# Performance work log

Hardware: AMD Instinct MI355X
Metric: run time of the kernel (lower is better)

Reference implementation:

```python
import jax, jax.numpy as jnp
import numpy as np

DIM = 576
HEADS = 8
AGENT = 49
GRID_SIZE = 5
ORDER = 3
BN_EPS = 1e-5


def _kan_grid():
    h = 2.0 / GRID_SIZE  # grid_range [-1, 1]
    return jnp.arange(-ORDER, GRID_SIZE + ORDER + 1, dtype=jnp.float32) * h - 1.0


def _bsplines(x, grid):
    # x: (M, in) -> (M, in, GRID_SIZE + ORDER) Cox-de Boor B-spline bases (efficient-kan)
    xe = x[..., None]
    b = ((xe >= grid[:-1]) & (xe < grid[1:])).astype(x.dtype)
    for k in range(1, ORDER + 1):
        b = ((xe - grid[:-(k + 1)]) / (grid[k:-1] - grid[:-(k + 1)]) * b[..., :-1]
             + (grid[k + 1:] - xe) / (grid[k + 1:] - grid[1:-k]) * b[..., 1:])
    return b


def setup_inputs() -> dict:
    key = jax.random.key(0)
    ks = jax.random.split(key, 16)
    b, H, W = 32, 28, 28
    n, c = H * W, DIM
    nrm = lambda k, shape, std=0.02: jax.random.normal(k, shape, jnp.float32) * std
    return {
        "x": jax.random.normal(ks[0], (b, n, c), jnp.float32),
        "H": H,
        "W": W,
        "Wq": nrm(ks[1], (c, c)),
        "Wkv": nrm(ks[2], (2 * c, c)),
        "an_bias": nrm(ks[3], (HEADS, AGENT, 7, 7)),
        "na_bias": nrm(ks[4], (HEADS, AGENT, 7, 7)),
        "ah_bias": nrm(ks[5], (1, HEADS, AGENT, H, 1)),
        "aw_bias": nrm(ks[6], (1, HEADS, AGENT, 1, W)),
        "ha_bias": nrm(ks[7], (1, HEADS, H, 1, AGENT)),
        "wa_bias": nrm(ks[8], (1, HEADS, 1, W, AGENT)),
        "dwc_w": nrm(ks[9], (c, 1, 3, 3), 0.1),
        "dwc_b": jnp.zeros((c,), jnp.float32),
        "bn_gamma": jnp.ones((c,), jnp.float32),
        "bn_beta": jnp.zeros((c,), jnp.float32),
        "bn_mean": jnp.zeros((c,), jnp.float32),
        "bn_var": jnp.ones((c,), jnp.float32),
        "base_weight": nrm(ks[10], (c, c)),
        "spline_weight": nrm(ks[11], (c, c, GRID_SIZE + ORDER)),
        "spline_scaler": jnp.ones((c, c), jnp.float32),
    }


def reference(x, H, W, Wq, Wkv, an_bias, na_bias, ah_bias, aw_bias, ha_bias, wa_bias,
              dwc_w, dwc_b, bn_gamma, bn_beta, bn_mean, bn_var,
              base_weight, spline_weight, spline_scaler):
    b, n, c = x.shape
    h, hd = HEADS, c // HEADS
    scale = hd ** -0.5
    q = x @ Wq.T                       # (b,n,c)
    kv = x @ Wkv.T                     # (b,n,2c)  (sr_ratio == 1)
    k, v = kv[..., :c], kv[..., c:]
    # agent tokens: AdaptiveAvgPool2d(28x28 -> 7x7) == exact 4x4 mean pooling
    p = int(AGENT ** 0.5)
    agent = q.reshape(b, p, H // p, p, W // p, c).mean(axis=(2, 4)).reshape(b, AGENT, c)
    qh = q.reshape(b, n, h, hd).transpose(0, 2, 1, 3)       # (b,h,n,hd)
    kh = k.reshape(b, n, h, hd).transpose(0, 2, 1, 3)
    vh = v.reshape(b, n, h, hd).transpose(0, 2, 1, 3)
    ah = agent.reshape(b, AGENT, h, hd).transpose(0, 2, 1, 3)  # (b,h,A,hd)
    # stage 1: agent tokens attend to k/v (bilinear-upsampled 7x7 bias + separable bias)
    pb1 = jax.image.resize(an_bias, (h, AGENT, H, W), "bilinear").reshape(1, h, AGENT, n)
    pb2 = (ah_bias + aw_bias).reshape(1, h, AGENT, n)
    agent_attn = jax.nn.softmax(jnp.einsum("bhad,bhnd->bhan", ah * scale, kh) + pb1 + pb2, axis=-1)
    agent_v = jnp.einsum("bhan,bhnd->bhad", agent_attn, vh)    # (b,h,A,hd)
    # stage 2: queries attend to agent tokens
    ab1 = jax.image.resize(na_bias, (h, AGENT, H, W), "bilinear").reshape(1, h, AGENT, n).transpose(0, 1, 3, 2)
    ab2 = (ha_bias + wa_bias).reshape(1, h, n, AGENT)
    q_attn = jax.nn.softmax(jnp.einsum("bhnd,bhad->bhna", qh * scale, ah) + ab1 + ab2, axis=-1)
    out = jnp.einsum("bhna,bhad->bhnd", q_attn, agent_v).transpose(0, 2, 1, 3).reshape(b, n, c)
    # depthwise-conv + BN(eval) + ReLU residual on v
    vimg = v.transpose(0, 2, 1).reshape(b, c, H, W)
    y = jax.lax.conv_general_dilated(vimg, dwc_w, (1, 1), "SAME",
                                     feature_group_count=c,
                                     dimension_numbers=("NCHW", "OIHW", "NCHW"))
    y = y + dwc_b[None, :, None, None]
    scale_bn = (bn_gamma / jnp.sqrt(bn_var + BN_EPS))[None, :, None, None]
    y = (y - bn_mean[None, :, None, None]) * scale_bn + bn_beta[None, :, None, None]
    y = jax.nn.relu(y).reshape(b, c, n).transpose(0, 2, 1)
    out = out + y
    # KANLinear projection: silu base branch + B-spline branch
    xf = out.reshape(b * n, c)
    bases = _bsplines(xf, _kan_grid())                           # (M, in, 8)
    scaled = spline_weight * spline_scaler[..., None]            # (out, in, 8)
    proj = jax.nn.silu(xf) @ base_weight.T + jnp.einsum("mik,oik->mo", bases, scaled)
    return proj.reshape(b, n, c)
```

## Files before the change

### kernel.cpp

```cpp
#include <hip/hip_runtime.h>
#include <hip/hip_bf16.h>
#include <math.h>

#define B_ 32
#define N_ 784
#define C_ 576
#define H_ 28
#define W_ 28
#define HEADS_ 8
#define HD_ 72
#define AGENT_ 49
#define M_ (B_ * N_)
#define KTOT_ 5184
#define QKVW_ 1728
#define SCALE_ 0.11785113019775793f

#define SWZ(row, chunk) (((row) << 5) + ((((chunk) ^ (((row) >> 1) & 3))) << 3))

typedef unsigned short ushort_t;
typedef __attribute__((ext_vector_type(8))) unsigned short u16x8;
typedef __attribute__((ext_vector_type(8))) __bf16 bf16x8;
typedef __attribute__((ext_vector_type(4))) float f32x4;
typedef __attribute__((ext_vector_type(4))) unsigned u32x4;

__device__ __forceinline__ ushort_t f2bf(float f) {
  union { float f; unsigned u; } v; v.f = f;
  unsigned r = v.u + 0x7fffu + ((v.u >> 16) & 1u);
  return (ushort_t)(r >> 16);
}
__device__ __forceinline__ float bf2f(ushort_t u) {
  union { unsigned u; float f; } v; v.u = ((unsigned)u) << 16;
  return v.f;
}
__device__ __forceinline__ unsigned pack2(float lo, float hi) {
  __bf16 a = (__bf16)lo, b = (__bf16)hi;
  unsigned short ua = __builtin_bit_cast(unsigned short, a);
  unsigned short ub = __builtin_bit_cast(unsigned short, b);
  return (unsigned)ua | ((unsigned)ub << 16);
}

__global__ __launch_bounds__(256) void convert_x_kernel(
    const float* __restrict__ x, ushort_t* __restrict__ xbf) {
  const int total8 = M_ * C_ / 8;
  for (int i = blockIdx.x * 256 + threadIdx.x; i < total8; i += gridDim.x * 256) {
    f32x4 a = *(const f32x4*)(x + i * 8);
    f32x4 b = *(const f32x4*)(x + i * 8 + 4);
    u16x8 o;
    o[0]=f2bf(a[0]); o[1]=f2bf(a[1]); o[2]=f2bf(a[2]); o[3]=f2bf(a[3]);
    o[4]=f2bf(b[0]); o[5]=f2bf(b[1]); o[6]=f2bf(b[2]); o[7]=f2bf(b[3]);
    *(u16x8*)(xbf + i * 8) = o;
  }
}

__global__ __launch_bounds__(256) void pack_w_kernel(
    const float* __restrict__ Wq, const float* __restrict__ Wkv,
    ushort_t* __restrict__ wbf) {
  int total = QKVW_ * C_;
  for (int i = blockIdx.x * 256 + threadIdx.x; i < total; i += gridDim.x * 256) {
    int j = i / C_, k = i % C_;
    float v = (j < C_) ? Wq[(size_t)j * C_ + k] : Wkv[(size_t)(j - C_) * C_ + k];
    wbf[i] = f2bf(v);
  }
}

__global__ __launch_bounds__(256) void pack_b_kernel(
    const float* __restrict__ base_w, const float* __restrict__ spline_w,
    const float* __restrict__ spline_s, ushort_t* __restrict__ bpackb) {
  int o = blockIdx.x;
  for (int j = threadIdx.x; j < KTOT_; j += 256) {
    float v;
    if (j < C_) {
      v = base_w[(size_t)o * C_ + j];
    } else {
      int jj = j - C_;
      int i = jj >> 3, kk = jj & 7;
      v = spline_w[((size_t)o * C_ + i) * 8 + kk] * spline_s[(size_t)o * C_ + i];
    }
    bpackb[(size_t)o * KTOT_ + j] = f2bf(v);
  }
}

__device__ __forceinline__ float bilerp7(const float* __restrict__ Bsrc, int y, int x) {
  float sy = y * 0.25f - 0.375f;
  float sx = x * 0.25f - 0.375f;
  float fy0 = floorf(sy), fx0 = floorf(sx);
  int y0 = (int)fy0, x0 = (int)fx0;
  float fy = sy - fy0, fx = sx - fx0;
  int y0c = min(6, max(0, y0)), y1c = min(6, max(0, y0 + 1));
  int x0c = min(6, max(0, x0)), x1c = min(6, max(0, x0 + 1));
  float v00 = Bsrc[y0c * 7 + x0c], v01 = Bsrc[y0c * 7 + x1c];
  float v10 = Bsrc[y1c * 7 + x0c], v11 = Bsrc[y1c * 7 + x1c];
  return (1.f - fy) * ((1.f - fx) * v00 + fx * v01)
       + fy * ((1.f - fx) * v10 + fx * v11);
}

__global__ __launch_bounds__(256) void bias_kernel(
    const float* __restrict__ an_bias, const float* __restrict__ na_bias,
    const float* __restrict__ ah_bias, const float* __restrict__ aw_bias,
    const float* __restrict__ ha_bias, const float* __restrict__ wa_bias,
    float* __restrict__ abias, float* __restrict__ qbias) {
  int idx = blockIdx.x * 256 + threadIdx.x;
  if (idx >= HEADS_ * AGENT_ * N_) return;
  int n = idx % N_;
  int ha = idx / N_;
  int h = ha / AGENT_, a = ha % AGENT_;
  int y = n / W_, x = n % W_;
  float pb1 = bilerp7(an_bias + (size_t)ha * 49, y, x);
  float pb2 = ah_bias[ha * H_ + y] + aw_bias[ha * W_ + x];
  abias[(size_t)ha * N_ + n] = pb1 + pb2;
  float ab1 = bilerp7(na_bias + (size_t)ha * 49, y, x);
  float ab2 = ha_bias[(h * H_ + y) * AGENT_ + a] + wa_bias[(h * W_ + x) * AGENT_ + a];
  qbias[((size_t)h * N_ + n) * AGENT_ + a] = ab1 + ab2;
}

__global__ __launch_bounds__(256, 4) void mfma_qkv_kernel(
    const ushort_t* __restrict__ A, const ushort_t* __restrict__ Bt,
    ushort_t* __restrict__ out) {
  __shared__ ushort_t Asl[2][128 * 32];
  __shared__ ushort_t Bsl[2][96 * 32];
  const int tid = threadIdx.x;
  const int lane = tid & 63, wid = tid >> 6;
  const int wm = wid >> 1, wn = wid & 1;
  const int l16 = lane & 15, lq = lane >> 4;

  int lin = blockIdx.x;
  int xcd = lin & 7;
  int wg = xcd * 441 + (lin >> 3);
  const int m0 = (wg / 18) * 128, n0 = (wg % 18) * 96;

  const int rA = tid >> 2, hA = tid & 3;
  const int rB0 = tid >> 2, cB0 = tid & 3;
  const int rB1 = 64 + (tid >> 2);
  const bool hasB1 = tid < 128;

  const ushort_t* arow0 = A + (size_t)(m0 + rA) * C_ + hA * 8;
  const ushort_t* arow1 = arow0 + (size_t)64 * C_;
  const ushort_t* brow0 = Bt + (size_t)(n0 + rB0) * C_ + cB0 * 8;
  const ushort_t* brow1 = Bt + (size_t)(n0 + rB1) * C_ + cB0 * 8;

  const int aWo0 = SWZ(rA, hA), aWo1 = SWZ(rA + 64, hA);
  const int b0Wo = SWZ(rB0, cB0), b1Wo = SWZ(rB1, cB0);

  f32x4 acc[4][3] = {};
  u16x8 ar0, ar1, br0, br1;

  ar0 = *(const u16x8*)(arow0);
  ar1 = *(const u16x8*)(arow1);
  br0 = *(const u16x8*)(brow0);
  if (hasB1) br1 = *(const u16x8*)(brow1);
  *(u16x8*)&Asl[0][aWo0] = ar0;
  *(u16x8*)&Asl[0][aWo1] = ar1;
  *(u16x8*)&Bsl[0][b0Wo] = br0;
  if (hasB1) *(u16x8*)&Bsl[0][b1Wo] = br1;
  ar0 = *(const u16x8*)(arow0 + 32);
  ar1 = *(const u16x8*)(arow1 + 32);
  br0 = *(const u16x8*)(brow0 + 32);
  if (hasB1) br1 = *(const u16x8*)(brow1 + 32);
  __syncthreads();

  const int NSTEP = C_ / 32;
  for (int s = 0; s < NSTEP; ++s) {
    const int cur = s & 1;
    bf16x8 af[4], bfr[3];
    #pragma unroll
    for (int fm = 0; fm < 4; ++fm)
      af[fm] = *(const bf16x8*)&Asl[cur][SWZ(wm * 64 + fm * 16 + l16, lq)];
    #pragma unroll
    for (int fn = 0; fn < 3; ++fn)
      bfr[fn] = *(const bf16x8*)&Bsl[cur][SWZ(wn * 48 + fn * 16 + l16, lq)];
    #pragma unroll
    for (int fm = 0; fm < 4; ++fm)
      #pragma unroll
      for (int fn = 0; fn < 3; ++fn)
        acc[fm][fn] = __builtin_amdgcn_mfma_f32_16x16x32_bf16(
            af[fm], bfr[fn], acc[fm][fn], 0, 0, 0);
    if (s + 1 < NSTEP) {
      const int nxt = cur ^ 1;
      *(u16x8*)&Asl[nxt][aWo0] = ar0;
      *(u16x8*)&Asl[nxt][aWo1] = ar1;
      *(u16x8*)&Bsl[nxt][b0Wo] = br0;
      if (hasB1) *(u16x8*)&Bsl[nxt][b1Wo] = br1;
      if (s + 2 < NSTEP) {
        const int kl = (s + 2) * 32;
        ar0 = *(const u16x8*)(arow0 + kl);
        ar1 = *(const u16x8*)(arow1 + kl);
        br0 = *(const u16x8*)(brow0 + kl);
        if (hasB1) br1 = *(const u16x8*)(brow1 + kl);
      }
    }
    __syncthreads();
  }
  #pragma unroll
  for (int fm = 0; fm < 4; ++fm) {
    #pragma unroll
    for (int fn = 0; fn < 3; ++fn) {
      int col = n0 + wn * 48 + fn * 16 + l16;
      #pragma unroll
      for (int r2 = 0; r2 < 4; ++r2) {
        int row = m0 + wm * 64 + fm * 16 + lq * 4 + r2;
        out[(size_t)row * QKVW_ + col] = f2bf(acc[fm][fn][r2]);
      }
    }
  }
}

__device__ __forceinline__ u32x4 basesPack(float xv) {
  float s = __fmaf_rn(xv, 2.5f, 5.5f);
  float tf = floorf(s);
  int t = (int)tf;
  float u = s - tf;
  float u2 = u * u, u3 = u2 * u, um = 1.f - u;
  float p0 = u3 * (1.f / 6.f);
  float p1 = __fmaf_rn(u3, -0.5f, __fmaf_rn(u2, 0.5f, __fmaf_rn(u, 0.5f, 1.f / 6.f)));
  float p2 = __fmaf_rn(u3, 0.5f, __fmaf_rn(u2, -1.f, 2.f / 3.f));
  float p3 = um * um * um * (1.f / 6.f);
  unsigned lo = pack2(p3, p2);
  unsigned hi = pack2(p1, p0);
  unsigned long long packed = ((unsigned long long)hi << 32) | (unsigned long long)lo;
  int sh = t - 3;
  int ba = sh << 4;
  unsigned long long shl_lo = packed << (ba & 63);
  unsigned long long shr_sp = packed >> ((64 - ba) & 63);
  unsigned long long shl_hi = packed << ((ba - 64) & 63);
  unsigned long long shr_ng = packed >> ((-ba) & 63);
  unsigned long long Olo = (sh < 0) ? shr_ng : ((sh < 4) ? shl_lo : 0ull);
  unsigned long long Ohi = (sh <= 0) ? 0ull : ((sh < 4) ? shr_sp : shl_hi);
  if (t < 0 || t > 10) { Olo = 0ull; Ohi = 0ull; }
  u32x4 o;
  o[0] = (unsigned)Olo; o[1] = (unsigned)(Olo >> 32);
  o[2] = (unsigned)Ohi; o[3] = (unsigned)(Ohi >> 32);
  return o;
}

__device__ __forceinline__ u32x4 siluPack(const float* xv) {
  u32x4 o;
  #pragma unroll
  for (int e = 0; e < 4; ++e) {
    float v0 = xv[2 * e], v1 = xv[2 * e + 1];
    float s0 = v0 / (1.f + __expf(-v0));
    float s1 = v1 / (1.f + __expf(-v1));
    o[e] = pack2(s0, s1);
  }
  return o;
}

__global__ __launch_bounds__(256, 4) void kan_mfma_kernel(
    const float* __restrict__ xf, const ushort_t* __restrict__ Bt,
    float* __restrict__ out) {
  __shared__ ushort_t Asl[2][128 * 32];
  __shared__ ushort_t Bsl[2][96 * 32];
  const int tid = threadIdx.x;
  const int lane = tid & 63, wid = tid >> 6;
  const int wm = wid >> 1, wn = wid & 1;
  const int l16 = lane & 15, lq = lane >> 4;

  int lin = blockIdx.x;
  int xcd = lin & 7;
  int wg = xcd * 147 + (lin >> 3);
  const int m0 = (wg / 6) * 128, n0 = (wg % 6) * 96;

  const int rA = tid >> 2, hA = tid & 3;
  const int rB0 = tid >> 2, cB0 = tid & 3;
  const int rB1 = 64 + (tid >> 2);
  const bool hasB1 = tid < 128;

  const float* xfr0 = xf + (size_t)(m0 + rA) * C_;
  const float* xfr1 = xfr0 + (size_t)64 * C_;
  const ushort_t* brow0 = Bt + (size_t)(n0 + rB0) * KTOT_ + cB0 * 8;
  const ushort_t* brow1 = Bt + (size_t)(n0 + rB1) * KTOT_ + cB0 * 8;

  const int aWo0 = SWZ(rA, hA), aWo1 = SWZ(rA + 64, hA);
  const int b0Wo = SWZ(rB0, cB0), b1Wo = SWZ(rB1, cB0);

  f32x4 acc[4][3] = {};
  float xv0[8], xv1[8];
  u16x8 br0, br1;

  {
    f32x4 a = *(const f32x4*)(xfr0 + hA * 8);
    f32x4 b = *(const f32x4*)(xfr0 + hA * 8 + 4);
    xv0[0]=a[0]; xv0[1]=a[1]; xv0[2]=a[2]; xv0[3]=a[3];
    xv0[4]=b[0]; xv0[5]=b[1]; xv0[6]=b[2]; xv0[7]=b[3];
    f32x4 c = *(const f32x4*)(xfr1 + hA * 8);
    f32x4 d = *(const f32x4*)(xfr1 + hA * 8 + 4);
    xv1[0]=c[0]; xv1[1]=c[1]; xv1[2]=c[2]; xv1[3]=c[3];
    xv1[4]=d[0]; xv1[5]=d[1]; xv1[6]=d[2]; xv1[7]=d[3];
  }
  br0 = *(const u16x8*)(brow0);
  if (hasB1) br1 = *(const u16x8*)(brow1);
  *(u32x4*)&Asl[0][aWo0] = siluPack(xv0);
  *(u32x4*)&Asl[0][aWo1] = siluPack(xv1);
  *(u16x8*)&Bsl[0][b0Wo] = br0;
  if (hasB1) *(u16x8*)&Bsl[0][b1Wo] = br1;
  {
    f32x4 a = *(const f32x4*)(xfr0 + 32 + hA * 8);
    f32x4 b = *(const f32x4*)(xfr0 + 32 + hA * 8 + 4);
    xv0[0]=a[0]; xv0[1]=a[1]; xv0[2]=a[2]; xv0[3]=a[3];
    xv0[4]=b[0]; xv0[5]=b[1]; xv0[6]=b[2]; xv0[7]=b[3];
    f32x4 c = *(const f32x4*)(xfr1 + 32 + hA * 8);
    f32x4 d = *(const f32x4*)(xfr1 + 32 + hA * 8 + 4);
    xv1[0]=c[0]; xv1[1]=c[1]; xv1[2]=c[2]; xv1[3]=c[3];
    xv1[4]=d[0]; xv1[5]=d[1]; xv1[6]=d[2]; xv1[7]=d[3];
  }
  br0 = *(const u16x8*)(brow0 + 32);
  if (hasB1) br1 = *(const u16x8*)(brow1 + 32);
  __syncthreads();

  const int NSTEP = KTOT_ / 32;
  for (int s = 0; s < NSTEP; ++s) {
    const int cur = s & 1;
    bf16x8 af[4], bfr[3];
    #pragma unroll
    for (int fm = 0; fm < 4; ++fm)
      af[fm] = *(const bf16x8*)&Asl[cur][SWZ(wm * 64 + fm * 16 + l16, lq)];
    #pragma unroll
    for (int fn = 0; fn < 3; ++fn)
      bfr[fn] = *(const bf16x8*)&Bsl[cur][SWZ(wn * 48 + fn * 16 + l16, lq)];
    #pragma unroll
    for (int fm = 0; fm < 4; ++fm)
      #pragma unroll
      for (int fn = 0; fn < 3; ++fn)
        acc[fm][fn] = __builtin_amdgcn_mfma_f32_16x16x32_bf16(
            af[fm], bfr[fn], acc[fm][fn], 0, 0, 0);
    if (s + 1 < NSTEP) {
      const int nxt = cur ^ 1;
      const int kg = (s + 1) * 32;
      u32x4 a0, a1;
      if (kg < C_) { a0 = siluPack(xv0); a1 = siluPack(xv1); }
      else         { a0 = basesPack(xv0[0]); a1 = basesPack(xv1[0]); }
      *(u32x4*)&Asl[nxt][aWo0] = a0;
      *(u32x4*)&Asl[nxt][aWo1] = a1;
      *(u16x8*)&Bsl[nxt][b0Wo] = br0;
      if (hasB1) *(u16x8*)&Bsl[nxt][b1Wo] = br1;
      if (s + 2 < NSTEP) {
        const int kl = (s + 2) * 32;
        if (kl < C_) {
          f32x4 a = *(const f32x4*)(xfr0 + kl + hA * 8);
          f32x4 b = *(const f32x4*)(xfr0 + kl + hA * 8 + 4);
          xv0[0]=a[0]; xv0[1]=a[1]; xv0[2]=a[2]; xv0[3]=a[3];
          xv0[4]=b[0]; xv0[5]=b[1]; xv0[6]=b[2]; xv0[7]=b[3];
          f32x4 c = *(const f32x4*)(xfr1 + kl + hA * 8);
          f32x4 d = *(const f32x4*)(xfr1 + kl + hA * 8 + 4);
          xv1[0]=c[0]; xv1[1]=c[1]; xv1[2]=c[2]; xv1[3]=c[3];
          xv1[4]=d[0]; xv1[5]=d[1]; xv1[6]=d[2]; xv1[7]=d[3];
        } else {
          int i0 = ((kl - C_) >> 3) + hA;
          xv0[0] = xfr0[i0];
          xv1[0] = xfr1[i0];
        }
        br0 = *(const u16x8*)(brow0 + kl);
        if (hasB1) br1 = *(const u16x8*)(brow1 + kl);
      }
    }
    __syncthreads();
  }
  #pragma unroll
  for (int fm = 0; fm < 4; ++fm) {
    #pragma unroll
    for (int fn = 0; fn < 3; ++fn) {
      int col = n0 + wn * 48 + fn * 16 + l16;
      #pragma unroll
      for (int r2 = 0; r2 < 4; ++r2) {
        int row = m0 + wm * 64 + fm * 16 + lq * 4 + r2;
        out[(size_t)row * C_ + col] = acc[fm][fn][r2];
      }
    }
  }
}

__global__ __launch_bounds__(576) void agent_pool_kernel(
    const ushort_t* __restrict__ qkvb, float* __restrict__ agent) {
  int ba = blockIdx.x;
  int b = ba / AGENT_, a = ba % AGENT_;
  int ay = a / 7, ax = a % 7;
  int ch = threadIdx.x;
  float s = 0.f;
  #pragma unroll
  for (int i2 = 0; i2 < 4; ++i2)
    #pragma unroll
    for (int i4 = 0; i4 < 4; ++i4)
      s += bf2f(qkvb[((size_t)b * N_ + (ay * 4 + i2) * W_ + (ax * 4 + i4)) * QKVW_ + ch]);
  agent[(size_t)ba * C_ + ch] = s * 0.0625f;
}

#define AKS_ 104
#define VTS_ 136
__global__ __launch_bounds__(256) void agent_attn_mfma_kernel(
    const float* __restrict__ agent, const ushort_t* __restrict__ qkvb,
    const float* __restrict__ abias, float* __restrict__ agent_v) {
  __shared__ ushort_t A_lds[64 * AKS_];
  __shared__ ushort_t K_lds[112 * AKS_];
  __shared__ ushort_t Vt_lds[80 * VTS_];
  __shared__ ushort_t P_lds[4][16 * VTS_];
  const int tid = threadIdx.x;
  const int lane = tid & 63, wid = tid >> 6;
  const int l16 = lane & 15, lq = lane >> 4;
  const int b = blockIdx.x >> 3, h = blockIdx.x & 7;

  for (int i = tid; i < 64 * AKS_; i += 256) A_lds[i] = 0;
  for (int i = tid; i < 112 * 32; i += 256) {
    int r = i >> 5, cc = 72 + (i & 31);
    K_lds[r * AKS_ + cc] = 0;
  }
  for (int i = tid; i < 80 * VTS_; i += 256) Vt_lds[i] = 0;
  for (int i = tid; i < 4 * 16 * 24; i += 256) {
    int w = i / (16 * 24), rest = i % (16 * 24);
    int r = rest / 24, cc = 112 + rest % 24;
    P_lds[w][r * VTS_ + cc] = 0;
  }
  for (int i = tid; i < AGENT_ * HD_; i += 256) {
    int a = i / HD_, d = i % HD_;
    A_lds[a * AKS_ + d] = f2bf(agent[((size_t)b * AGENT_ + a) * C_ + h * HD_ + d]);
  }

  int srow[4], scol[4]; bool sval[4];
  #pragma unroll
  for (int i = 0; i < 4; ++i) {
    int idx = tid + i * 256;
    srow[i] = idx / 9; scol[i] = idx % 9;
    sval[i] = idx < 1008;
  }
  const ushort_t* kbase = qkvb + (size_t)b * N_ * QKVW_ + C_ + h * HD_;
  const ushort_t* vbase = qkvb + (size_t)b * N_ * QKVW_ + 2 * C_ + h * HD_;

  u16x8 kreg[4], vreg[4];
  #pragma unroll
  for (int i = 0; i < 4; ++i) {
    if (sval[i]) {
      kreg[i] = *(const u16x8*)(kbase + (size_t)srow[i] * QKVW_ + scol[i] * 8);
      vreg[i] = *(const u16x8*)(vbase + (size_t)srow[i] * QKVW_ + scol[i] * 8);
    }
  }
  #pragma unroll
  for (int i = 0; i < 4; ++i) {
    if (sval[i]) {
      *(u16x8*)&K_lds[srow[i] * AKS_ + scol[i] * 8] = kreg[i];
      #pragma unroll
      for (int e = 0; e < 8; ++e)
        Vt_lds[(scol[i] * 8 + e) * VTS_ + srow[i]] = vreg[i][e];
    }
  }
  __syncthreads();

  float m_r[4] = {-1e30f, -1e30f, -1e30f, -1e30f};
  float l_r[4] = {};
  f32x4 O[5] = {};
  const float* bias_base[4];
  #pragma unroll
  for (int r = 0; r < 4; ++r) {
    int a = wid * 16 + lq * 4 + r;
    a = min(a, AGENT_ - 1);
    bias_base[r] = abias + ((size_t)h * AGENT_ + a) * N_;
  }

  for (int c = 0; c < 7; ++c) {
    if (c < 6) {
      const size_t off = (size_t)(c + 1) * 112 * QKVW_;
      #pragma unroll
      for (int i = 0; i < 4; ++i) {
        if (sval[i]) {
          kreg[i] = *(const u16x8*)(kbase + off + (size_t)srow[i] * QKVW_ + scol[i] * 8);
          vreg[i] = *(const u16x8*)(vbase + off + (size_t)srow[i] * QKVW_ + scol[i] * 8);
        }
      }
    }
    f32x4 sacc[7] = {};
    #pragma unroll
    for (int ks = 0; ks < 3; ++ks) {
      bf16x8 af = *(const bf16x8*)&A_lds[(wid * 16 + l16) * AKS_ + ks * 32 + lq * 8];
      #pragma unroll
      for (int nt = 0; nt < 7; ++nt) {
        bf16x8 bf = *(const bf16x8*)&K_lds[(nt * 16 + l16) * AKS_ + ks * 32 + lq * 8];
        sacc[nt] = __builtin_amdgcn_mfma_f32_16x16x32_bf16(af, bf, sacc[nt], 0, 0, 0);
      }
    }
    float cmax[4] = {-1e30f, -1e30f, -1e30f, -1e30f};
    const int nb = c * 112 + l16;
    #pragma unroll
    for (int nt = 0; nt < 7; ++nt)
      #pragma unroll
      for (int r = 0; r < 4; ++r) {
        float lg = sacc[nt][r] * SCALE_ + bias_base[r][nb + nt * 16];
        sacc[nt][r] = lg;
        cmax[r] = fmaxf(cmax[r], lg);
      }
    #pragma unroll
    for (int off = 1; off < 16; off <<= 1)
      #pragma unroll
      for (int r = 0; r < 4; ++r)
        cmax[r] = fmaxf(cmax[r], __shfl_xor(cmax[r], off));
    float scl[4], rs[4];
    #pragma unroll
    for (int r = 0; r < 4; ++r) {
      float nm = fmaxf(m_r[r], cmax[r]);
      scl[r] = __expf(m_r[r] - nm);
      m_r[r] = nm;
      rs[r] = 0.f;
    }
    #pragma unroll
    for (int nt = 0; nt < 7; ++nt)
      #pragma unroll
      for (int r = 0; r < 4; ++r) {
        float p = __expf(sacc[nt][r] - m_r[r]);
        rs[r] += p;
        P_lds[wid][(lq * 4 + r) * VTS_ + nt * 16 + l16] = f2bf(p);
      }
    #pragma unroll
    for (int off = 1; off < 16; off <<= 1)
      #pragma unroll
      for (int r = 0; r < 4; ++r)
        rs[r] += __shfl_xor(rs[r], off);
    #pragma unroll
    for (int r = 0; r < 4; ++r) l_r[r] = l_r[r] * scl[r] + rs[r];
    #pragma unroll
    for (int nt = 0; nt < 5; ++nt)
      #pragma unroll
      for (int r = 0; r < 4; ++r) O[nt][r] *= scl[r];
    #pragma unroll
    for (int ks = 0; ks < 4; ++ks) {
      bf16x8 pf = *(const bf16x8*)&P_lds[wid][l16 * VTS_ + ks * 32 + lq * 8];
      #pragma unroll
      for (int nt = 0; nt < 5; ++nt) {
        bf16x8 vf = *(const bf16x8*)&Vt_lds[(nt * 16 + l16) * VTS_ + ks * 32 + lq * 8];
        O[nt] = __builtin_amdgcn_mfma_f32_16x16x32_bf16(pf, vf, O[nt], 0, 0, 0);
      }
    }
    __syncthreads();
    if (c < 6) {
      #pragma unroll
      for (int i = 0; i < 4; ++i) {
        if (sval[i]) {
          *(u16x8*)&K_lds[srow[i] * AKS_ + scol[i] * 8] = kreg[i];
          #pragma unroll
          for (int e = 0; e < 8; ++e)
            Vt_lds[(scol[i] * 8 + e) * VTS_ + srow[i]] = vreg[i][e];
        }
      }
      __syncthreads();
    }
  }
  float inv[4];
  #pragma unroll
  for (int r = 0; r < 4; ++r) inv[r] = 1.f / l_r[r];
  #pragma unroll
  for (int nt = 0; nt < 5; ++nt) {
    int d = nt * 16 + l16;
    if (d >= HD_) continue;
    #pragma unroll
    for (int r = 0; r < 4; ++r) {
      int a = wid * 16 + lq * 4 + r;
      if (a < AGENT_)
        agent_v[(((size_t)b * HEADS_ + h) * AGENT_ + a) * HD_ + d] = O[nt][r] * inv[r];
    }
  }
}

__global__ __launch_bounds__(256) void q_attn_kernel(
    const ushort_t* __restrict__ qkvb, const float* __restrict__ agent,
    const float* __restrict__ agent_v, const float* __restrict__ qbias,
    float* __restrict__ xf) {
  __shared__ float ag_t[HD_ * 52];
  __shared__ float av_t[HD_ * 52];
  const int tid = threadIdx.x;
  const int h = blockIdx.y, b = blockIdx.z;
  for (int t = tid; t < AGENT_ * HD_; t += 256) {
    int a = t / HD_, d = t % HD_;
    ag_t[d * 52 + a] = agent[((size_t)b * AGENT_ + a) * C_ + h * HD_ + d];
    av_t[d * 52 + a] = agent_v[(((size_t)b * HEADS_ + h) * AGENT_ + a) * HD_ + d];
  }
  __syncthreads();
  const int n = blockIdx.x * 256 + tid;
  if (n >= N_) return;
  const ushort_t* qp = qkvb + ((size_t)b * N_ + n) * QKVW_ + h * HD_;
  const float* qb = qbias + ((size_t)h * N_ + n) * AGENT_;
  float lg[AGENT_];
  #pragma unroll
  for (int a = 0; a < AGENT_; ++a) lg[a] = qb[a];
  for (int d = 0; d < HD_; ++d) {
    float qd = bf2f(qp[d]) * SCALE_;
    #pragma unroll
    for (int a = 0; a < AGENT_; ++a) lg[a] += qd * ag_t[d * 52 + a];
  }
  float mx = -1e30f;
  #pragma unroll
  for (int a = 0; a < AGENT_; ++a) mx = fmaxf(mx, lg[a]);
  float s = 0.f;
  #pragma unroll
  for (int a = 0; a < AGENT_; ++a) { lg[a] = __expf(lg[a] - mx); s += lg[a]; }
  float inv = 1.f / s;
  #pragma unroll
  for (int a = 0; a < AGENT_; ++a) lg[a] *= inv;
  float* op = xf + ((size_t)b * N_ + n) * C_ + h * HD_;
  for (int d = 0; d < HD_; ++d) {
    float acc = 0.f;
    #pragma unroll
    for (int a = 0; a < AGENT_; ++a) acc += lg[a] * av_t[d * 52 + a];
    op[d] = acc;
  }
}

__global__ __launch_bounds__(288) void dwc_kernel(
    const ushort_t* __restrict__ qkvb, const float* __restrict__ w,
    const float* __restrict__ bias, const float* __restrict__ gamma,
    const float* __restrict__ beta, const float* __restrict__ mean,
    const float* __restrict__ var, float* __restrict__ xf) {
  int lin = blockIdx.x;
  const int bn = (lin & 7) * 3136 + (lin >> 3);
  const int b = bn / N_, n = bn % N_;
  const int y = n / W_, x = n % W_;
  const int c0 = threadIdx.x * 2;
  float a0 = 0.f, a1 = 0.f;
  #pragma unroll
  for (int ky = 0; ky < 3; ++ky) {
    int yy = y + ky - 1;
    if (yy < 0 || yy >= H_) continue;
    #pragma unroll
    for (int kx = 0; kx < 3; ++kx) {
      int xx = x + kx - 1;
      if (xx < 0 || xx >= W_) continue;
      unsigned v = *(const unsigned*)(qkvb + ((size_t)b * N_ + yy * W_ + xx) * QKVW_ + 2 * C_ + c0);
      a0 += w[c0 * 9 + ky * 3 + kx] * bf2f((ushort_t)(v & 0xffffu));
      a1 += w[(c0 + 1) * 9 + ky * 3 + kx] * bf2f((ushort_t)(v >> 16));
    }
  }
  float s0 = gamma[c0] * rsqrtf(var[c0] + 1e-5f);
  float s1 = gamma[c0 + 1] * rsqrtf(var[c0 + 1] + 1e-5f);
  float r0 = fmaxf((a0 + bias[c0] - mean[c0]) * s0 + beta[c0], 0.f);
  float r1 = fmaxf((a1 + bias[c0 + 1] - mean[c0 + 1]) * s1 + beta[c0 + 1], 0.f);
  float2* xp = (float2*)&xf[(size_t)bn * C_ + c0];
  float2 old = *xp;
  old.x += r0; old.y += r1;
  *xp = old;
}

extern "C" void kernel_launch(void* const* d_in, const int* in_sizes, int n_in,
                              void* d_out, int out_size, void* d_ws, size_t ws_size,
                              hipStream_t stream) {
  const float* x        = (const float*)d_in[0];
  const float* Wq       = (const float*)d_in[3];
  const float* Wkv      = (const float*)d_in[4];
  const float* an_bias  = (const float*)d_in[5];
  const float* na_bias  = (const float*)d_in[6];
  const float* ah_bias  = (const float*)d_in[7];
  const float* aw_bias  = (const float*)d_in[8];
  const float* ha_bias  = (const float*)d_in[9];
  const float* wa_bias  = (const float*)d_in[10];
  const float* dwc_w    = (const float*)d_in[11];
  const float* dwc_b    = (const float*)d_in[12];
  const float* bn_gamma = (const float*)d_in[13];
  const float* bn_beta  = (const float*)d_in[14];
  const float* bn_mean  = (const float*)d_in[15];
  const float* bn_var   = (const float*)d_in[16];
  const float* base_w   = (const float*)d_in[17];
  const float* spline_w = (const float*)d_in[18];
  const float* spline_s = (const float*)d_in[19];

  char* ws = (char*)d_ws;
  ushort_t* qkvb   = (ushort_t*)(ws + 0);
  ushort_t* xbf    = (ushort_t*)(ws + 86704128);
  ushort_t* wbf    = (ushort_t*)(ws + 115605504);
  ushort_t* bpackb = (ushort_t*)(ws + 117596160);
  float* agent     = (float*)(ws + 123568128);
  float* agent_v   = (float*)(ws + 127180800);
  float* abias     = (float*)(ws + 130793472);
  float* qbias     = (float*)(ws + 132022784);
  float* xf        = (float*)(ws + 133252096);
  float* out       = (float*)d_out;

  convert_x_kernel<<<dim3(2048), dim3(256), 0, stream>>>(x, xbf);
  pack_w_kernel<<<dim3(1024), dim3(256), 0, stream>>>(Wq, Wkv, wbf);
  pack_b_kernel<<<dim3(C_), dim3(256), 0, stream>>>(base_w, spline_w, spline_s, bpackb);
  bias_kernel<<<dim3((HEADS_ * AGENT_ * N_ + 255) / 256), dim3(256), 0, stream>>>(
      an_bias, na_bias, ah_bias, aw_bias, ha_bias, wa_bias, abias, qbias);
  mfma_qkv_kernel<<<dim3(3528), dim3(256), 0, stream>>>(xbf, wbf, qkvb);
  agent_pool_kernel<<<dim3(B_ * AGENT_), dim3(C_), 0, stream>>>(qkvb, agent);
  agent_attn_mfma_kernel<<<dim3(B_ * HEADS_), dim3(256), 0, stream>>>(
      agent, qkvb, abias, agent_v);
  q_attn_kernel<<<dim3(4, HEADS_, B_), dim3(256), 0, stream>>>(
      qkvb, agent, agent_v, qbias, xf);
  dwc_kernel<<<dim3(M_), dim3(288), 0, stream>>>(
      qkvb, dwc_w, dwc_b, bn_gamma, bn_beta, bn_mean, bn_var, xf);
  kan_mfma_kernel<<<dim3(1176), dim3(256), 0, stream>>>(xf, bpackb, out);
}
```

Baseline: 682.7 us.

## Enlarge GEMM tiles to 128x192 with K-step 64 and 8 waves per block

```diff
diff --git a/kernel.cpp b/kernel.cpp
--- a/kernel.cpp
+++ b/kernel.cpp
@@ -15,7 +15,7 @@
 #define QKVW_ 1728
 #define SCALE_ 0.11785113019775793f
 
-#define SWZ(row, chunk) (((row) << 5) + ((((chunk) ^ (((row) >> 1) & 3))) << 3))
+#define SWZ64(row, chunk) (((row) << 6) + ((((chunk) ^ ((row) & 7))) << 3))
 
 typedef unsigned short ushort_t;
 typedef __attribute__((ext_vector_type(8))) unsigned short u16x8;
@@ -113,79 +113,88 @@
   qbias[((size_t)h * N_ + n) * AGENT_ + a] = ab1 + ab2;
 }
 
-__global__ __launch_bounds__(256, 4) void mfma_qkv_kernel(
+__global__ __launch_bounds__(512, 4) void mfma_qkv_kernel(
     const ushort_t* __restrict__ A, const ushort_t* __restrict__ Bt,
     ushort_t* __restrict__ out) {
-  __shared__ ushort_t Asl[2][128 * 32];
-  __shared__ ushort_t Bsl[2][96 * 32];
+  __shared__ ushort_t Asl[2][128 * 64];
+  __shared__ ushort_t Bsl[2][192 * 64];
   const int tid = threadIdx.x;
   const int lane = tid & 63, wid = tid >> 6;
-  const int wm = wid >> 1, wn = wid & 1;
+  const int wm = wid >> 2, wn = wid & 3;
   const int l16 = lane & 15, lq = lane >> 4;
 
   int lin = blockIdx.x;
+  const int q = 220, r = 4;
   int xcd = lin & 7;
-  int wg = xcd * 441 + (lin >> 3);
-  const int m0 = (wg / 18) * 128, n0 = (wg % 18) * 96;
-
-  const int rA = tid >> 2, hA = tid & 3;
-  const int rB0 = tid >> 2, cB0 = tid & 3;
-  const int rB1 = 64 + (tid >> 2);
-  const bool hasB1 = tid < 128;
-
-  const ushort_t* arow0 = A + (size_t)(m0 + rA) * C_ + hA * 8;
+  int wg = (xcd < r ? xcd * (q + 1) : r * (q + 1) + (xcd - r) * q) + (lin >> 3);
+  const int m0 = (wg / 9) * 128, n0 = (wg % 9) * 192;
+
+  const int srowi = tid >> 3;
+  const int chk = tid & 7;
+
+  const ushort_t* arow0 = A + (size_t)(m0 + srowi) * C_ + chk * 8;
   const ushort_t* arow1 = arow0 + (size_t)64 * C_;
-  const ushort_t* brow0 = Bt + (size_t)(n0 + rB0) * C_ + cB0 * 8;
-  const ushort_t* brow1 = Bt + (size_t)(n0 + rB1) * C_ + cB0 * 8;
-
-  const int aWo0 = SWZ(rA, hA), aWo1 = SWZ(rA + 64, hA);
-  const int b0Wo = SWZ(rB0, cB0), b1Wo = SWZ(rB1, cB0);
+  const ushort_t* brow0 = Bt + (size_t)(n0 + srowi) * C_ + chk * 8;
+  const ushort_t* brow1 = brow0 + (size_t)64 * C_;
+  const ushort_t* brow2 = brow0 + (size_t)128 * C_;
+
+  const int aW0 = SWZ64(srowi, chk), aW1 = SWZ64(srowi + 64, chk);
+  const int bW0 = SWZ64(srowi, chk), bW1 = SWZ64(srowi + 64, chk),
+            bW2 = SWZ64(srowi + 128, chk);
 
   f32x4 acc[4][3] = {};
-  u16x8 ar0, ar1, br0, br1;
+  u16x8 ar0, ar1, br0, br1, br2;
 
   ar0 = *(const u16x8*)(arow0);
   ar1 = *(const u16x8*)(arow1);
   br0 = *(const u16x8*)(brow0);
-  if (hasB1) br1 = *(const u16x8*)(brow1);
-  *(u16x8*)&Asl[0][aWo0] = ar0;
-  *(u16x8*)&Asl[0][aWo1] = ar1;
-  *(u16x8*)&Bsl[0][b0Wo] = br0;
-  if (hasB1) *(u16x8*)&Bsl[0][b1Wo] = br1;
-  ar0 = *(const u16x8*)(arow0 + 32);
-  ar1 = *(const u16x8*)(arow1 + 32);
-  br0 = *(const u16x8*)(brow0 + 32);
-  if (hasB1) br1 = *(const u16x8*)(brow1 + 32);
+  br1 = *(const u16x8*)(brow1);
+  br2 = *(const u16x8*)(brow2);
+  *(u16x8*)&Asl[0][aW0] = ar0;
+  *(u16x8*)&Asl[0][aW1] = ar1;
+  *(u16x8*)&Bsl[0][bW0] = br0;
+  *(u16x8*)&Bsl[0][bW1] = br1;
+  *(u16x8*)&Bsl[0][bW2] = br2;
+  ar0 = *(const u16x8*)(arow0 + 64);
+  ar1 = *(const u16x8*)(arow1 + 64);
+  br0 = *(const u16x8*)(brow0 + 64);
+  br1 = *(const u16x8*)(brow1 + 64);
+  br2 = *(const u16x8*)(brow2 + 64);
   __syncthreads();
 
-  const int NSTEP = C_ / 32;
+  const int NSTEP = C_ / 64;
   for (int s = 0; s < NSTEP; ++s) {
     const int cur = s & 1;
-    bf16x8 af[4], bfr[3];
-    #pragma unroll
-    for (int fm = 0; fm < 4; ++fm)
-      af[fm] = *(const bf16x8*)&Asl[cur][SWZ(wm * 64 + fm * 16 + l16, lq)];
-    #pragma unroll
-    for (int fn = 0; fn < 3; ++fn)
-      bfr[fn] = *(const bf16x8*)&Bsl[cur][SWZ(wn * 48 + fn * 16 + l16, lq)];
-    #pragma unroll
-    for (int fm = 0; fm < 4; ++fm)
+    #pragma unroll
+    for (int ks = 0; ks < 2; ++ks) {
+      bf16x8 af[4], bfr[3];
+      #pragma unroll
+      for (int fm = 0; fm < 4; ++fm)
+        af[fm] = *(const bf16x8*)&Asl[cur][SWZ64(wm * 64 + fm * 16 + l16, ks * 4 + lq)];
       #pragma unroll
       for (int fn = 0; fn < 3; ++fn)
-        acc[fm][fn] = __builtin_amdgcn_mfma_f32_16x16x32_bf16(
-            af[fm], bfr[fn], acc[fm][fn], 0, 0, 0);
+        bfr[fn] = *(const bf16x8*)&Bsl[cur][SWZ64(wn * 48 + fn * 16 + l16, ks * 4 + lq)];
+      #pragma unroll
+      for (int fm = 0; fm < 4; ++fm)
+        #pragma unroll
+        for (int fn = 0; fn < 3; ++fn)
+          acc[fm][fn] = __builtin_amdgcn_mfma_f32_16x16x32_bf16(
+              af[fm], bfr[fn], acc[fm][fn], 0, 0, 0);
+    }
     if (s + 1 < NSTEP) {
       const int nxt = cur ^ 1;
-      *(u16x8*)&Asl[nxt][aWo0] = ar0;
-      *(u16x8*)&Asl[nxt][aWo1] = ar1;
-      *(u16x8*)&Bsl[nxt][b0Wo] = br0;
-      if (hasB1) *(u16x8*)&Bsl[nxt][b1Wo] = br1;
+      *(u16x8*)&Asl[nxt][aW0] = ar0;
+      *(u16x8*)&Asl[nxt][aW1] = ar1;
+      *(u16x8*)&Bsl[nxt][bW0] = br0;
+      *(u16x8*)&Bsl[nxt][bW1] = br1;
+      *(u16x8*)&Bsl[nxt][bW2] = br2;
       if (s + 2 < NSTEP) {
-        const int kl = (s + 2) * 32;
+        const int kl = (s + 2) * 64;
         ar0 = *(const u16x8*)(arow0 + kl);
         ar1 = *(const u16x8*)(arow1 + kl);
         br0 = *(const u16x8*)(brow0 + kl);
-        if (hasB1) br1 = *(const u16x8*)(brow1 + kl);
+        br1 = *(const u16x8*)(brow1 + kl);
+        br2 = *(const u16x8*)(brow2 + kl);
       }
     }
     __syncthreads();
@@ -244,112 +253,121 @@
   return o;
 }
 
-__global__ __launch_bounds__(256, 4) void kan_mfma_kernel(
+__global__ __launch_bounds__(512, 4) void kan_mfma_kernel(
     const float* __restrict__ xf, const ushort_t* __restrict__ Bt,
     float* __restrict__ out) {
-  __shared__ ushort_t Asl[2][128 * 32];
-  __shared__ ushort_t Bsl[2][96 * 32];
+  __shared__ ushort_t Asl[2][128 * 64];
+  __shared__ ushort_t Bsl[2][192 * 64];
   const int tid = threadIdx.x;
   const int lane = tid & 63, wid = tid >> 6;
-  const int wm = wid >> 1, wn = wid & 1;
+  const int wm = wid >> 2, wn = wid & 3;
   const int l16 = lane & 15, lq = lane >> 4;
 
   int lin = blockIdx.x;
+  const int q = 73, r = 4;
   int xcd = lin & 7;
-  int wg = xcd * 147 + (lin >> 3);
-  const int m0 = (wg / 6) * 128, n0 = (wg % 6) * 96;
-
-  const int rA = tid >> 2, hA = tid & 3;
-  const int rB0 = tid >> 2, cB0 = tid & 3;
-  const int rB1 = 64 + (tid >> 2);
-  const bool hasB1 = tid < 128;
-
-  const float* xfr0 = xf + (size_t)(m0 + rA) * C_;
+  int wg = (xcd < r ? xcd * (q + 1) : r * (q + 1) + (xcd - r) * q) + (lin >> 3);
+  const int m0 = (wg / 3) * 128, n0 = (wg % 3) * 192;
+
+  const int srowi = tid >> 3;
+  const int chk = tid & 7;
+
+  const float* xfr0 = xf + (size_t)(m0 + srowi) * C_;
   const float* xfr1 = xfr0 + (size_t)64 * C_;
-  const ushort_t* brow0 = Bt + (size_t)(n0 + rB0) * KTOT_ + cB0 * 8;
-  const ushort_t* brow1 = Bt + (size_t)(n0 + rB1) * KTOT_ + cB0 * 8;
-
-  const int aWo0 = SWZ(rA, hA), aWo1 = SWZ(rA + 64, hA);
-  const int b0Wo = SWZ(rB0, cB0), b1Wo = SWZ(rB1, cB0);
+  const ushort_t* brow0 = Bt + (size_t)(n0 + srowi) * KTOT_ + chk * 8;
+  const ushort_t* brow1 = brow0 + (size_t)64 * KTOT_;
+  const ushort_t* brow2 = brow0 + (size_t)128 * KTOT_;
+
+  const int aW0 = SWZ64(srowi, chk), aW1 = SWZ64(srowi + 64, chk);
+  const int bW0 = SWZ64(srowi, chk), bW1 = SWZ64(srowi + 64, chk),
+            bW2 = SWZ64(srowi + 128, chk);
 
   f32x4 acc[4][3] = {};
   float xv0[8], xv1[8];
-  u16x8 br0, br1;
+  u16x8 br0, br1, br2;
 
   {
-    f32x4 a = *(const f32x4*)(xfr0 + hA * 8);
-    f32x4 b = *(const f32x4*)(xfr0 + hA * 8 + 4);
+    f32x4 a = *(const f32x4*)(xfr0 + chk * 8);
+    f32x4 b = *(const f32x4*)(xfr0 + chk * 8 + 4);
     xv0[0]=a[0]; xv0[1]=a[1]; xv0[2]=a[2]; xv0[3]=a[3];
     xv0[4]=b[0]; xv0[5]=b[1]; xv0[6]=b[2]; xv0[7]=b[3];
-    f32x4 c = *(const f32x4*)(xfr1 + hA * 8);
-    f32x4 d = *(const f32x4*)(xfr1 + hA * 8 + 4);
+    f32x4 c = *(const f32x4*)(xfr1 + chk * 8);
+    f32x4 d = *(const f32x4*)(xfr1 + chk * 8 + 4);
     xv1[0]=c[0]; xv1[1]=c[1]; xv1[2]=c[2]; xv1[3]=c[3];
     xv1[4]=d[0]; xv1[5]=d[1]; xv1[6]=d[2]; xv1[7]=d[3];
   }
   br0 = *(const u16x8*)(brow0);
-  if (hasB1) br1 = *(const u16x8*)(brow1);
-  *(u32x4*)&Asl[0][aWo0] = siluPack(xv0);
-  *(u32x4*)&Asl[0][aWo1] = siluPack(xv1);
-  *(u16x8*)&Bsl[0][b0Wo] = br0;
-  if (hasB1) *(u16x8*)&Bsl[0][b1Wo] = br1;
+  br1 = *(const u16x8*)(brow1);
+  br2 = *(const u16x8*)(brow2);
+  *(u32x4*)&Asl[0][aW0] = siluPack(xv0);
+  *(u32x4*)&Asl[0][aW1] = siluPack(xv1);
+  *(u16x8*)&Bsl[0][bW0] = br0;
+  *(u16x8*)&Bsl[0][bW1] = br1;
+  *(u16x8*)&Bsl[0][bW2] = br2;
   {
-    f32x4 a = *(const f32x4*)(xfr0 + 32 + hA * 8);
-    f32x4 b = *(const f32x4*)(xfr0 + 32 + hA * 8 + 4);
+    f32x4 a = *(const f32x4*)(xfr0 + 64 + chk * 8);
+    f32x4 b = *(const f32x4*)(xfr0 + 64 + chk * 8 + 4);
     xv0[0]=a[0]; xv0[1]=a[1]; xv0[2]=a[2]; xv0[3]=a[3];
     xv0[4]=b[0]; xv0[5]=b[1]; xv0[6]=b[2]; xv0[7]=b[3];
-    f32x4 c = *(const f32x4*)(xfr1 + 32 + hA * 8);
-    f32x4 d = *(const f32x4*)(xfr1 + 32 + hA * 8 + 4);
+    f32x4 c = *(const f32x4*)(xfr1 + 64 + chk * 8);
+    f32x4 d = *(const f32x4*)(xfr1 + 64 + chk * 8 + 4);
     xv1[0]=c[0]; xv1[1]=c[1]; xv1[2]=c[2]; xv1[3]=c[3];
     xv1[4]=d[0]; xv1[5]=d[1]; xv1[6]=d[2]; xv1[7]=d[3];
   }
-  br0 = *(const u16x8*)(brow0 + 32);
-  if (hasB1) br1 = *(const u16x8*)(brow1 + 32);
+  br0 = *(const u16x8*)(brow0 + 64);
+  br1 = *(const u16x8*)(brow1 + 64);
+  br2 = *(const u16x8*)(brow2 + 64);
   __syncthreads();
 
-  const int NSTEP = KTOT_ / 32;
+  const int NSTEP = KTOT_ / 64;
   for (int s = 0; s < NSTEP; ++s) {
     const int cur = s & 1;
-    bf16x8 af[4], bfr[3];
-    #pragma unroll
-    for (int fm = 0; fm < 4; ++fm)
-      af[fm] = *(const bf16x8*)&Asl[cur][SWZ(wm * 64 + fm * 16 + l16, lq)];
-    #pragma unroll
-    for (int fn = 0; fn < 3; ++fn)
-      bfr[fn] = *(const bf16x8*)&Bsl[cur][SWZ(wn * 48 + fn * 16 + l16, lq)];
-    #pragma unroll
-    for (int fm = 0; fm < 4; ++fm)
+    #pragma unroll
+    for (int ks = 0; ks < 2; ++ks) {
+      bf16x8 af[4], bfr[3];
+      #pragma unroll
+      for (int fm = 0; fm < 4; ++fm)
+        af[fm] = *(const bf16x8*)&Asl[cur][SWZ64(wm * 64 + fm * 16 + l16, ks * 4 + lq)];
       #pragma unroll
       for (int fn = 0; fn < 3; ++fn)
-        acc[fm][fn] = __builtin_amdgcn_mfma_f32_16x16x32_bf16(
-            af[fm], bfr[fn], acc[fm][fn], 0, 0, 0);
+        bfr[fn] = *(const bf16x8*)&Bsl[cur][SWZ64(wn * 48 + fn * 16 + l16, ks * 4 + lq)];
+      #pragma unroll
+      for (int fm = 0; fm < 4; ++fm)
+        #pragma unroll
+        for (int fn = 0; fn < 3; ++fn)
+          acc[fm][fn] = __builtin_amdgcn_mfma_f32_16x16x32_bf16(
+              af[fm], bfr[fn], acc[fm][fn], 0, 0, 0);
+    }
     if (s + 1 < NSTEP) {
       const int nxt = cur ^ 1;
-      const int kg = (s + 1) * 32;
+      const int kg = (s + 1) * 64;
       u32x4 a0, a1;
       if (kg < C_) { a0 = siluPack(xv0); a1 = siluPack(xv1); }
       else         { a0 = basesPack(xv0[0]); a1 = basesPack(xv1[0]); }
-      *(u32x4*)&Asl[nxt][aWo0] = a0;
-      *(u32x4*)&Asl[nxt][aWo1] = a1;
-      *(u16x8*)&Bsl[nxt][b0Wo] = br0;
-      if (hasB1) *(u16x8*)&Bsl[nxt][b1Wo] = br1;
+      *(u32x4*)&Asl[nxt][aW0] = a0;
+      *(u32x4*)&Asl[nxt][aW1] = a1;
+      *(u16x8*)&Bsl[nxt][bW0] = br0;
+      *(u16x8*)&Bsl[nxt][bW1] = br1;
+      *(u16x8*)&Bsl[nxt][bW2] = br2;
       if (s + 2 < NSTEP) {
-        const int kl = (s + 2) * 32;
+        const int kl = (s + 2) * 64;
         if (kl < C_) {
-          f32x4 a = *(const f32x4*)(xfr0 + kl + hA * 8);
-          f32x4 b = *(const f32x4*)(xfr0 + kl + hA * 8 + 4);
+          f32x4 a = *(const f32x4*)(xfr0 + kl + chk * 8);
+          f32x4 b = *(const f32x4*)(xfr0 + kl + chk * 8 + 4);
           xv0[0]=a[0]; xv0[1]=a[1]; xv0[2]=a[2]; xv0[3]=a[3];
           xv0[4]=b[0]; xv0[5]=b[1]; xv0[6]=b[2]; xv0[7]=b[3];
-          f32x4 c = *(const f32x4*)(xfr1 + kl + hA * 8);
-          f32x4 d = *(const f32x4*)(xfr1 + kl + hA * 8 + 4);
+          f32x4 c = *(const f32x4*)(xfr1 + kl + chk * 8);
+          f32x4 d = *(const f32x4*)(xfr1 + kl + chk * 8 + 4);
           xv1[0]=c[0]; xv1[1]=c[1]; xv1[2]=c[2]; xv1[3]=c[3];
           xv1[4]=d[0]; xv1[5]=d[1]; xv1[6]=d[2]; xv1[7]=d[3];
         } else {
-          int i0 = ((kl - C_) >> 3) + hA;
+          int i0 = ((kl - C_) >> 3) + chk;
           xv0[0] = xfr0[i0];
           xv1[0] = xfr1[i0];
         }
         br0 = *(const u16x8*)(brow0 + kl);
-        if (hasB1) br1 = *(const u16x8*)(brow1 + kl);
+        br1 = *(const u16x8*)(brow1 + kl);
+        br2 = *(const u16x8*)(brow2 + kl);
       }
     }
     __syncthreads();
@@ -672,7 +690,7 @@
   pack_b_kernel<<<dim3(C_), dim3(256), 0, stream>>>(base_w, spline_w, spline_s, bpackb);
   bias_kernel<<<dim3((HEADS_ * AGENT_ * N_ + 255) / 256), dim3(256), 0, stream>>>(
       an_bias, na_bias, ah_bias, aw_bias, ha_bias, wa_bias, abias, qbias);
-  mfma_qkv_kernel<<<dim3(3528), dim3(256), 0, stream>>>(xbf, wbf, qkvb);
+  mfma_qkv_kernel<<<dim3(1764), dim3(512), 0, stream>>>(xbf, wbf, qkvb);
   agent_pool_kernel<<<dim3(B_ * AGENT_), dim3(C_), 0, stream>>>(qkvb, agent);
   agent_attn_mfma_kernel<<<dim3(B_ * HEADS_), dim3(256), 0, stream>>>(
       agent, qkvb, abias, agent_v);
@@ -680,5 +698,5 @@
       qkvb, agent, agent_v, qbias, xf);
   dwc_kernel<<<dim3(M_), dim3(288), 0, stream>>>(
       qkvb, dwc_w, dwc_b, bn_gamma, bn_beta, bn_mean, bn_var, xf);
-  kan_mfma_kernel<<<dim3(1176), dim3(256), 0, stream>>>(xf, bpackb, out);
-}
+  kan_mfma_kernel<<<dim3(588), dim3(512), 0, stream>>>(xf, bpackb, out);
+}
```

Measured after the change: 630.5 us. 7.6% less time.
